# Optimization experiments

Hardware: AMD Instinct MI355X
Metric: run time of the kernel (lower is better)

The kernel has to match this reference:

```python
import jax, jax.numpy as jnp
import numpy as np

B, N, F_IN, E, TOPK = 64, 1024, 64, 128, 32
NEG_SLOPE = 0.2  # GAT leaky-relu slope


def setup_inputs() -> dict:
    key = jax.random.key(0)
    ks = jax.random.split(key, 7)
    x = jax.random.normal(ks[0], (B, N, F_IN), dtype=jnp.float32)
    emb = jax.random.normal(ks[1], (N, E), dtype=jnp.float32)            # nn.Embedding table
    W_fe = jax.random.normal(ks[2], (F_IN, E), dtype=jnp.float32) / np.sqrt(F_IN).astype(np.float32)
    a_src = jax.random.normal(ks[3], (2 * E,), dtype=jnp.float32) * 0.05
    a_dst = jax.random.normal(ks[4], (2 * E,), dtype=jnp.float32) * 0.05
    lin_W = jax.random.normal(ks[5], (E, 1), dtype=jnp.float32) / np.sqrt(E).astype(np.float32)
    lin_b = jnp.zeros((1,), dtype=jnp.float32)
    return {"x": x, "emb": emb, "W_fe": W_fe, "a_src": a_src, "a_dst": a_dst,
            "lin_W": lin_W, "lin_b": lin_b}


def reference(x, emb, W_fe, a_src, a_dst, lin_W, lin_b):
    b, n, _ = x.shape
    e_dim = emb.shape[-1]
    # --- cosine-similarity topk graph construction (shared across batch) ---
    norm = jnp.linalg.norm(emb, axis=-1, keepdims=True)                  # [N,1]
    sim = (emb @ emb.T) / (norm @ norm.T)                                # [N,N]
    idx = jax.lax.top_k(sim, TOPK)[1]                                    # [N,K] int32 neighbor (target) nodes
    # --- graph attention feature extraction ---
    h = jnp.einsum('bnf,fe->bne', x, W_fe)                               # [B,N,E] projected node features
    g = jnp.concatenate([h, jnp.broadcast_to(emb, (b, n, e_dim))], -1)   # [B,N,2E] feat || embedding
    e_s = g @ a_src                                                      # [B,N] source attention term
    e_d = g @ a_dst                                                      # [B,N] target attention term
    # edges: source i repeated TOPK times -> targets idx[i]; softmax over each node's K neighbors
    scores = jax.nn.leaky_relu(e_s[:, :, None] + e_d[:, idx], NEG_SLOPE)  # [B,N,K]
    alpha = jax.nn.softmax(scores, axis=-1)                              # [B,N,K]
    h_dst = h[:, idx, :]                                                 # [B,N,K,E] gathered neighbor feats
    out = jnp.einsum('bnk,bnke->bne', alpha, h_dst)                      # aggregate messages
    out = jax.nn.relu(out)
    # --- linear readout ---
    y = out @ lin_W + lin_b                                              # [B,N,1]
    return y[..., 0]                                                     # [B,N]
```

## Files before the change

kernel.cpp:

```cpp
#include <hip/hip_runtime.h>
#include <math.h>

#define BB 64
#define NN 1024
#define F_IN 64
#define EE 128
#define TOPK 32
#define NEG_SLOPE 0.2f

typedef unsigned int uint;
typedef unsigned short ushort;
typedef unsigned long long ull;
typedef __attribute__((ext_vector_type(8))) short short8;
typedef __attribute__((ext_vector_type(4))) float f32x4;

static __device__ __forceinline__ uint f2bf(float f) {
  const uint x = __float_as_uint(f);
  return (x + 0x7fffu + ((x >> 16) & 1u)) >> 16;
}
static __device__ __forceinline__ float bf_lo(uint u) {
  return __uint_as_float(u << 16);
}
static __device__ __forceinline__ float bf_hi_raw(uint u) {
  return __uint_as_float(u);
}
static __device__ __forceinline__ uint fmono(float f) {
  uint u = __float_as_uint(f);
  return (u & 0x80000000u) ? ~u : (u | 0x80000000u);
}
static __device__ __forceinline__ ull umax64(ull a, ull b) {
  return a > b ? a : b;
}
static __device__ __forceinline__ ull umin64(ull a, ull b) {
  return a < b ? a : b;
}
static __device__ __forceinline__ ull shfl_xor64(ull v, int mask) {
  const uint lo = __shfl_xor((uint)v, mask);
  const uint hi = __shfl_xor((uint)(v >> 32), mask);
  return ((ull)hi << 32) | lo;
}

__global__ __launch_bounds__(256) void k2a_sim(
    const float* __restrict__ emb, const float* __restrict__ a_src,
    const float* __restrict__ a_dst, const float* __restrict__ W_fe,
    uint* __restrict__ keys, float* __restrict__ u_src,
    float* __restrict__ u_dst, ushort* __restrict__ wt) {
  __shared__ __align__(16) float ei[8][132];
  __shared__ __align__(16) float ej[64][132];
  const int t = threadIdx.x, wid = t >> 6, lane = t & 63;
  const int i0 = (blockIdx.x >> 2) * 8;
  const int jbase = (blockIdx.x & 3) * 256;

  if ((blockIdx.x & 3) == 0) {
    const int row = i0 + 2 * wid + (lane >> 5);
    const int ll = lane & 31;
    const float* er = emb + (size_t)row * EE;
    float us = 0.f, ud = 0.f;
#pragma unroll
    for (int c0 = 0; c0 < EE; c0 += 32) {
      const int c = c0 + ll;
      const float e = er[c];
      us += e * a_src[EE + c];
      ud += e * a_dst[EE + c];
    }
#pragma unroll
    for (int o = 1; o <= 16; o <<= 1) {
      us += __shfl_xor(us, o);
      ud += __shfl_xor(ud, o);
    }
    if (ll == 0) {
      u_src[row] = us;
      u_dst[row] = ud;
    }
  } else if ((blockIdx.x & 3) == 1 && (blockIdx.x >> 2) < 32) {
    const int g = (blockIdx.x >> 2) * 256 + t;
    const int n = g >> 6, k = g & 63;
    wt[g] = (ushort)f2bf(W_fe[k * EE + n]);
  }

  {
    const int r = t >> 5, c4 = t & 31;
    const float4 v = *(const float4*)&emb[(size_t)(i0 + r) * EE + c4 * 4];
    *(float4*)&ei[r][c4 * 4] = v;
  }

  const int ia = i0 + wid * 2;

  for (int ch = 0; ch < 4; ++ch) {
    const int j0 = jbase + ch * 64;
#pragma unroll
    for (int p = 0; p < 8; ++p) {
      const int g = p * 256 + t;
      const int r = g >> 5, c4 = g & 31;
      const float4 v = *(const float4*)&emb[(size_t)(j0 + r) * EE + c4 * 4];
      *(float4*)&ej[r][c4 * 4] = v;
    }
    __syncthreads();

    float a0 = 0.f, a1 = 0.f, sq = 0.f;
#pragma unroll 8
    for (int d4 = 0; d4 < 32; ++d4) {
      const float4 e = *(const float4*)&ej[lane][4 * d4];
      const float4 wa = *(const float4*)&ei[wid * 2][4 * d4];
      const float4 wb = *(const float4*)&ei[wid * 2 + 1][4 * d4];
      a0 += e.x * wa.x + e.y * wa.y + e.z * wa.z + e.w * wa.w;
      a1 += e.x * wb.x + e.y * wb.y + e.z * wb.z + e.w * wb.w;
      sq += e.x * e.x + e.y * e.y + e.z * e.z + e.w * e.w;
    }
    const int jg = j0 + lane;
    const float rj = rsqrtf(sq);
    keys[(size_t)ia * NN + jg] = fmono(a0 * rj);
    keys[(size_t)(ia + 1) * NN + jg] = fmono(a1 * rj);
    __syncthreads();
  }
}

__global__ __launch_bounds__(256) void k23(
    const uint* __restrict__ keys, int* __restrict__ idx_out,
    const float* __restrict__ x, const ushort* __restrict__ wt,
    const float* __restrict__ a_src, const float* __restrict__ a_dst,
    const float* __restrict__ u_src, const float* __restrict__ u_dst,
    uint* __restrict__ h2, float* __restrict__ es, float* __restrict__ ed) {
  __shared__ ull cand[128];
  const int t = threadIdx.x, wid = t >> 6, lane = t & 63;

  if (blockIdx.x < NN) {
    const int row = blockIdx.x;

    const int jb = wid * 256 + lane * 4;
    const uint4 kv = *(const uint4*)&keys[(size_t)row * NN + jb];
    ull xr[4];
    xr[0] = ((ull)kv.x << 32) | (uint)(jb + 0);
    xr[1] = ((ull)kv.y << 32) | (uint)(jb + 1);
    xr[2] = ((ull)kv.z << 32) | (uint)(jb + 2);
    xr[3] = ((ull)kv.w << 32) | (uint)(jb + 3);

#pragma unroll
    for (int k = 2; k <= 256; k <<= 1) {
#pragma unroll
      for (int d = 128; d >= 1; d >>= 1) {
        if (d > (k >> 1)) continue;
        if (d >= 4) {
          const int pl = d >> 2;
          const bool lower = (lane & pl) == 0;
#pragma unroll
          for (int r = 0; r < 4; ++r) {
            const ull o = shfl_xor64(xr[r], pl);
            const bool desc = (((lane * 4 + r) & k) == 0);
            const bool keepmax = (desc == lower);
            xr[r] = keepmax ? umax64(xr[r], o) : umin64(xr[r], o);
          }
        } else if (d == 2) {
#pragma unroll
          for (int r = 0; r < 2; ++r) {
            const bool desc = (((lane * 4 + r) & k) == 0);
            const ull hi = umax64(xr[r], xr[r + 2]);
            const ull lo = umin64(xr[r], xr[r + 2]);
            xr[r] = desc ? hi : lo;
            xr[r + 2] = desc ? lo : hi;
          }
        } else {
#pragma unroll
          for (int r = 0; r < 4; r += 2) {
            const bool desc = (((lane * 4 + r) & k) == 0);
            const ull hi = umax64(xr[r], xr[r + 1]);
            const ull lo = umin64(xr[r], xr[r + 1]);
            xr[r] = desc ? hi : lo;
            xr[r + 1] = desc ? lo : hi;
          }
        }
      }
    }
    if (lane < 8) {
#pragma unroll
      for (int r = 0; r < 4; ++r) cand[wid * 32 + lane * 4 + r] = xr[r];
    }
    __syncthreads();

    if (wid < 2) {
      const int base = wid * 64;
      ull v = (lane < 32) ? cand[base + lane] : cand[base + 95 - lane];
#pragma unroll
      for (int d = 32; d >= 1; d >>= 1) {
        const ull o = shfl_xor64(v, d);
        v = ((lane & d) == 0) ? umax64(v, o) : umin64(v, o);
      }
      if (lane < 32) cand[base + lane] = v;
    }
    __syncthreads();

    if (wid == 0) {
      ull v = (lane < 32) ? cand[lane] : cand[127 - lane];
#pragma unroll
      for (int d = 32; d >= 1; d >>= 1) {
        const ull o = shfl_xor64(v, d);
        v = ((lane & d) == 0) ? umax64(v, o) : umin64(v, o);
      }
      if (lane < 32) idx_out[(size_t)row * TOPK + lane] = (int)(v & 1023u);
    }
  } else {
    const int row0 = (blockIdx.x - NN) * 64;
    const int nn = lane & 15, quad = lane >> 4;
    const int row0w = row0 + wid * 16;

    short8 af[2];
#pragma unroll
    for (int s = 0; s < 2; ++s) {
      const float* xr2 = x + (size_t)(row0w + nn) * F_IN + s * 32 + quad * 8;
      const float4 v0 = *(const float4*)&xr2[0];
      const float4 v1 = *(const float4*)&xr2[4];
      af[s][0] = (short)f2bf(v0.x);
      af[s][1] = (short)f2bf(v0.y);
      af[s][2] = (short)f2bf(v0.z);
      af[s][3] = (short)f2bf(v0.w);
      af[s][4] = (short)f2bf(v1.x);
      af[s][5] = (short)f2bf(v1.y);
      af[s][6] = (short)f2bf(v1.z);
      af[s][7] = (short)f2bf(v1.w);
    }

    f32x4 acc[8];
#pragma unroll
    for (int T = 0; T < 8; ++T) acc[T] = (f32x4){0.f, 0.f, 0.f, 0.f};

#pragma unroll
    for (int T = 0; T < 8; ++T) {
#pragma unroll
      for (int s = 0; s < 2; ++s) {
        const short8 bf =
            *(const short8*)&wt[(T * 16 + nn) * F_IN + s * 32 + quad * 8];
        acc[T] =
            __builtin_amdgcn_mfma_f32_16x16x32_bf16(af[s], bf, acc[T], 0, 0, 0);
      }
    }

    const int growbase = row0w + quad * 4;
#pragma unroll
    for (int reg = 0; reg < 4; ++reg) {
      uint* hr = h2 + (size_t)(growbase + reg) * 64 + nn;
#pragma unroll
      for (int T4 = 0; T4 < 4; ++T4) {
        hr[T4 * 16] =
            f2bf(acc[2 * T4][reg]) | (f2bf(acc[2 * T4 + 1][reg]) << 16);
      }
    }
    float ae[8], de[8];
#pragma unroll
    for (int T = 0; T < 8; ++T) {
      ae[T] = a_src[T * 16 + nn];
      de[T] = a_dst[T * 16 + nn];
    }
#pragma unroll
    for (int reg = 0; reg < 4; ++reg) {
      float ps = 0.f, pd = 0.f;
#pragma unroll
      for (int T = 0; T < 8; ++T) {
        ps += acc[T][reg] * ae[T];
        pd += acc[T][reg] * de[T];
      }
#pragma unroll
      for (int o = 1; o <= 8; o <<= 1) {
        ps += __shfl_xor(ps, o);
        pd += __shfl_xor(pd, o);
      }
      if (nn == 0) {
        const int grow = growbase + reg;
        const int node = grow & (NN - 1);
        es[grow] = ps + u_src[node];
        ed[grow] = pd + u_dst[node];
      }
    }
  }
}

__global__ __launch_bounds__(256, 3) void k4_attn(
    const uint* __restrict__ h2, const float* __restrict__ es,
    const float* __restrict__ ed, const int* __restrict__ idx,
    const float* __restrict__ lin_W, const float* __restrict__ lin_b,
    float* __restrict__ y) {
  __shared__ uint2 pairs[16 * 34 + 2];
  const int t = threadIdx.x, wid = t >> 6, lane = t & 63;
  const int blk = blockIdx.x;
  const int xcd = blk & 7, xx = blk >> 3;
  const int b = xcd * 8 + (xx >> 6);
  const int q = lane >> 4, ll = lane & 15;
  const int n = (xx & 63) * 16 + wid * 4 + q;
  uint2* const pr = pairs + (wid * 4 + q) * 34;

  const float* edb = ed + (size_t)b * NN;
  const char* hb = (const char*)(h2 + (size_t)b * NN * 64);

  const int j0 = idx[n * TOPK + ll];
  const int j1 = idx[n * TOPK + 16 + ll];
  const float esv = es[(size_t)b * NN + n];
  float s0 = esv + edb[j0];
  float s1 = esv + edb[j1];
  s0 = s0 > 0.f ? s0 : NEG_SLOPE * s0;
  s1 = s1 > 0.f ? s1 : NEG_SLOPE * s1;
  const float p0 = __expf(s0);
  const float p1 = __expf(s1);
  uint2 st0, st1;
  st0.x = (uint)(j0 << 8);
  st0.y = __float_as_uint(p0);
  st1.x = (uint)(j1 << 8);
  st1.y = __float_as_uint(p1);
  pr[ll] = st0;
  pr[16 + ll] = st1;

  float lwlo[4], lwhi[4];
#pragma unroll
  for (int i = 0; i < 4; ++i) {
    const int c = 4 * ll + i;
    const int t4 = c >> 4, nn2 = c & 15;
    lwlo[i] = lin_W[t4 * 32 + nn2];
    lwhi[i] = lin_W[t4 * 32 + 16 + nn2];
  }
  const float bias = lin_b[0];

  float w[32];
  float acc[8];
#pragma unroll
  for (int i = 0; i < 8; ++i) acc[i] = 0.f;
  float dsum = 0.f;
  uint4 tvA[8], tvB[8];

#define LOADG(g, TV)                                                \
  {                                                                 \
    _Pragma("unroll") for (int k = 0; k < 8; ++k) {                 \
      const uint2 pw = pr[(g) * 8 + k];                             \
      w[(g) * 8 + k] = __uint_as_float(pw.y);                       \
      TV[k] = *(const uint4*)(hb + (pw.x + (uint)(ll * 16)));       \
    }                                                               \
  }
#define CONSG(g, TV)                                \
  {                                                 \
    _Pragma("unroll") for (int k = 0; k < 8; ++k) { \
      const float wk = w[(g) * 8 + k];              \
      dsum += wk;                                   \
      const uint4 u = TV[k];                        \
      acc[0] += wk * bf_lo(u.x);                    \
      acc[1] += wk * bf_hi_raw(u.x);                \
      acc[2] += wk * bf_lo(u.y);                    \
      acc[3] += wk * bf_hi_raw(u.y);                \
      acc[4] += wk * bf_lo(u.z);                    \
      acc[5] += wk * bf_hi_raw(u.z);                \
      acc[6] += wk * bf_lo(u.w);                    \
      acc[7] += wk * bf_hi_raw(u.w);                \
    }                                               \
  }

  LOADG(0, tvA)
  LOADG(1, tvB)
  CONSG(0, tvA)
  LOADG(2, tvA)
  CONSG(1, tvB)
  LOADG(3, tvB)
  CONSG(2, tvA)
  CONSG(3, tvB)
#undef LOADG
#undef CONSG

  const float rs = 1.0f / dsum;
  float r = 0.f;
#pragma unroll
  for (int i = 0; i < 4; ++i) {
    const float a0 = acc[2 * i] > 0.f ? acc[2 * i] : 0.f;
    const float a1 = acc[2 * i + 1] > 0.f ? acc[2 * i + 1] : 0.f;
    r += a0 * lwlo[i] + a1 * lwhi[i];
  }
#pragma unroll
  for (int o = 1; o <= 8; o <<= 1) r += __shfl_xor(r, o);
  if (ll == 0) y[(size_t)b * NN + n] = r * rs + bias;
}

extern "C" void kernel_launch(void* const* d_in, const int* in_sizes, int n_in,
                              void* d_out, int out_size, void* d_ws,
                              size_t ws_size, hipStream_t stream) {
  const float* x = (const float*)d_in[0];
  const float* emb = (const float*)d_in[1];
  const float* W_fe = (const float*)d_in[2];
  const float* a_src = (const float*)d_in[3];
  const float* a_dst = (const float*)d_in[4];
  const float* lin_W = (const float*)d_in[5];
  const float* lin_b = (const float*)d_in[6];
  float* y = (float*)d_out;

  char* ws = (char*)d_ws;
  float* u_src = (float*)(ws + 4096);
  float* u_dst = (float*)(ws + 8192);
  int* idx = (int*)(ws + 16384);
  float* es = (float*)(ws + 147456);
  float* ed = (float*)(ws + 409600);
  uint* h2 = (uint*)(ws + 671744);
  uint* keys = (uint*)(ws + 17448960);
  ushort* wt = (ushort*)(ws + 21643264);

  k2a_sim<<<512, 256, 0, stream>>>(emb, a_src, a_dst, W_fe, keys, u_src,
                                   u_dst, wt);
  k23<<<2048, 256, 0, stream>>>(keys, idx, x, wt, a_src, a_dst, u_src, u_dst,
                                h2, es, ed);
  k4_attn<<<4096, 256, 0, stream>>>(h2, es, ed, idx, lin_W, lin_b, y);
}
```

Baseline: 148.0 us.

## Remap attention kernel to 32 lanes per node with 8-byte gathers

The aggregation kernel now assigns 32 lanes to each node instead of 16. Each lane handles one neighbor's score and loads 8-byte slices of the neighbor feature rows. The denominator of the softmax is computed with a shuffle reduction, and all 32 gathers are issued up front behind a scheduling barrier. The grid doubles to keep total coverage the same. The aim is more memory-level parallelism and less per-lane work, at the cost of narrower loads and more blocks.

```diff
diff --git a/kernel.cpp b/kernel.cpp
--- a/kernel.cpp
+++ b/kernel.cpp
@@ -278,99 +278,69 @@
     const float* __restrict__ ed, const int* __restrict__ idx,
     const float* __restrict__ lin_W, const float* __restrict__ lin_b,
     float* __restrict__ y) {
-  __shared__ uint2 pairs[16 * 34 + 2];
-  const int t = threadIdx.x, wid = t >> 6, lane = t & 63;
+  __shared__ uint2 pairs[8 * 32];
+  const int t = threadIdx.x;
+  const int hw = t >> 5;
+  const int hl = t & 31;
   const int blk = blockIdx.x;
   const int xcd = blk & 7, xx = blk >> 3;
-  const int b = xcd * 8 + (xx >> 6);
-  const int q = lane >> 4, ll = lane & 15;
-  const int n = (xx & 63) * 16 + wid * 4 + q;
-  uint2* const pr = pairs + (wid * 4 + q) * 34;
-
-  const float* edb = ed + (size_t)b * NN;
+  const int b = xcd * 8 + (xx >> 7);
+  const int n = (xx & 127) * 8 + hw;
+
   const char* hb = (const char*)(h2 + (size_t)b * NN * 64);
 
-  const int j0 = idx[n * TOPK + ll];
-  const int j1 = idx[n * TOPK + 16 + ll];
+  const int j = idx[n * TOPK + hl];
   const float esv = es[(size_t)b * NN + n];
-  float s0 = esv + edb[j0];
-  float s1 = esv + edb[j1];
-  s0 = s0 > 0.f ? s0 : NEG_SLOPE * s0;
-  s1 = s1 > 0.f ? s1 : NEG_SLOPE * s1;
-  const float p0 = __expf(s0);
-  const float p1 = __expf(s1);
-  uint2 st0, st1;
-  st0.x = (uint)(j0 << 8);
-  st0.y = __float_as_uint(p0);
-  st1.x = (uint)(j1 << 8);
-  st1.y = __float_as_uint(p1);
-  pr[ll] = st0;
-  pr[16 + ll] = st1;
-
-  float lwlo[4], lwhi[4];
-#pragma unroll
-  for (int i = 0; i < 4; ++i) {
-    const int c = 4 * ll + i;
-    const int t4 = c >> 4, nn2 = c & 15;
-    lwlo[i] = lin_W[t4 * 32 + nn2];
-    lwhi[i] = lin_W[t4 * 32 + 16 + nn2];
+  float s = esv + ed[(size_t)b * NN + j];
+  s = s > 0.f ? s : NEG_SLOPE * s;
+  const float p = __expf(s);
+  float dsum = p;
+#pragma unroll
+  for (int o = 1; o <= 16; o <<= 1) dsum += __shfl_xor(dsum, o);
+  const float rs = 1.0f / dsum;
+
+  uint2 st;
+  st.x = (uint)(j << 8);
+  st.y = __float_as_uint(p);
+  pairs[hw * 32 + hl] = st;
+  const uint* prw = (const uint*)(pairs + hw * 32);
+
+  float lw[4];
+#pragma unroll
+  for (int m = 0; m < 2; ++m) {
+    const int u = hl * 2 + m;
+    const int T4 = u >> 4, nn2 = u & 15;
+    lw[2 * m] = lin_W[T4 * 32 + nn2];
+    lw[2 * m + 1] = lin_W[T4 * 32 + 16 + nn2];
   }
   const float bias = lin_b[0];
 
-  float w[32];
-  float acc[8];
-#pragma unroll
-  for (int i = 0; i < 8; ++i) acc[i] = 0.f;
-  float dsum = 0.f;
-  uint4 tvA[8], tvB[8];
-
-#define LOADG(g, TV)                                                \
-  {                                                                 \
-    _Pragma("unroll") for (int k = 0; k < 8; ++k) {                 \
-      const uint2 pw = pr[(g) * 8 + k];                             \
-      w[(g) * 8 + k] = __uint_as_float(pw.y);                       \
-      TV[k] = *(const uint4*)(hb + (pw.x + (uint)(ll * 16)));       \
-    }                                                               \
-  }
-#define CONSG(g, TV)                                \
-  {                                                 \
-    _Pragma("unroll") for (int k = 0; k < 8; ++k) { \
-      const float wk = w[(g) * 8 + k];              \
-      dsum += wk;                                   \
-      const uint4 u = TV[k];                        \
-      acc[0] += wk * bf_lo(u.x);                    \
-      acc[1] += wk * bf_hi_raw(u.x);                \
-      acc[2] += wk * bf_lo(u.y);                    \
-      acc[3] += wk * bf_hi_raw(u.y);                \
-      acc[4] += wk * bf_lo(u.z);                    \
-      acc[5] += wk * bf_hi_raw(u.z);                \
-      acc[6] += wk * bf_lo(u.w);                    \
-      acc[7] += wk * bf_hi_raw(u.w);                \
-    }                                               \
-  }
-
-  LOADG(0, tvA)
-  LOADG(1, tvB)
-  CONSG(0, tvA)
-  LOADG(2, tvA)
-  CONSG(1, tvB)
-  LOADG(3, tvB)
-  CONSG(2, tvA)
-  CONSG(3, tvB)
-#undef LOADG
-#undef CONSG
-
-  const float rs = 1.0f / dsum;
-  float r = 0.f;
-#pragma unroll
-  for (int i = 0; i < 4; ++i) {
-    const float a0 = acc[2 * i] > 0.f ? acc[2 * i] : 0.f;
-    const float a1 = acc[2 * i + 1] > 0.f ? acc[2 * i + 1] : 0.f;
-    r += a0 * lwlo[i] + a1 * lwhi[i];
-  }
-#pragma unroll
-  for (int o = 1; o <= 8; o <<= 1) r += __shfl_xor(r, o);
-  if (ll == 0) y[(size_t)b * NN + n] = r * rs + bias;
+  uint2 tv[32];
+#pragma unroll
+  for (int k = 0; k < 32; ++k) {
+    const uint off = prw[2 * k];
+    tv[k] = *(const uint2*)(hb + (off + (uint)(hl * 8)));
+  }
+  __builtin_amdgcn_sched_barrier(0);
+
+  float acc0 = 0.f, acc1 = 0.f, acc2 = 0.f, acc3 = 0.f;
+#pragma unroll
+  for (int k = 0; k < 32; ++k) {
+    const float wk = __uint_as_float(prw[2 * k + 1]);
+    const uint2 u = tv[k];
+    acc0 += wk * bf_lo(u.x);
+    acc1 += wk * bf_hi_raw(u.x);
+    acc2 += wk * bf_lo(u.y);
+    acc3 += wk * bf_hi_raw(u.y);
+  }
+
+  float r = (acc0 > 0.f ? acc0 : 0.f) * lw[0] +
+            (acc1 > 0.f ? acc1 : 0.f) * lw[1] +
+            (acc2 > 0.f ? acc2 : 0.f) * lw[2] +
+            (acc3 > 0.f ? acc3 : 0.f) * lw[3];
+#pragma unroll
+  for (int o = 1; o <= 16; o <<= 1) r += __shfl_xor(r, o);
+  if (hl == 0) y[(size_t)b * NN + n] = r * rs + bias;
 }
 
 extern "C" void kernel_launch(void* const* d_in, const int* in_sizes, int n_in,
@@ -399,5 +369,5 @@
                                    u_dst, wt);
   k23<<<2048, 256, 0, stream>>>(keys, idx, x, wt, a_src, a_dst, u_src, u_dst,
                                 h2, es, ed);
-  k4_attn<<<4096, 256, 0, stream>>>(h2, es, ed, idx, lin_W, lin_b, y);
-}
+  k4_attn<<<8192, 256, 0, stream>>>(h2, es, ed, idx, lin_W, lin_b, y);
+}
```

New measurement: 147.6 us. About the same (-0.3%).
